# Kernel optimization log

Measured on AMD Instinct MI355X. Metric: run time of the kernel, lower is better.

Reference implementation:

```python
import jax, jax.numpy as jnp
from jax import lax
import numpy as np

B_SZ, L, NH, DH, DS = 2, 2048, 24, 64, 128


def setup_inputs() -> dict:
    key = jax.random.key(0)
    k1, k2, k3, k4 = jax.random.split(key, 4)
    x = jax.random.normal(k1, (B_SZ, L, NH, DH), dtype=jnp.float32)
    A = jax.random.normal(k2, (B_SZ, L, NH), dtype=jnp.float32)
    B_mat = jax.random.normal(k3, (B_SZ, L, NH, DS), dtype=jnp.float32)
    C_mat = jax.random.normal(k4, (B_SZ, L, NH, DS), dtype=jnp.float32)
    delta_param = jnp.zeros((NH,), dtype=jnp.float32)
    return {"x": x, "A": A, "B_mat": B_mat, "C_mat": C_mat, "delta_param": delta_param}


def reference(x, A, B_mat, C_mat, delta_param):
    # x: (B, L, nh, dh); A: (B, L, nh); B_mat/C_mat: (B, L, nh, ds)
    b, l, nh, dh = x.shape
    ds = B_mat.shape[-1]
    delta = jax.nn.softplus(A + delta_param[None, None, :])        # (B, L, nh)
    A_bar = jnp.exp(-delta * jnp.abs(A))                            # (B, L, nh)

    def step(h, inp):
        x_t, B_t, C_t, a_t = inp  # (B,nh,dh), (B,nh,ds), (B,nh,ds), (B,nh)
        h = a_t[:, :, None, None] * h + x_t[..., None] * B_t[:, :, None, :]
        y_t = jnp.einsum('bhds,bhs->bhd', h, C_t)                   # (B, nh, dh)
        return h, y_t

    h0 = jnp.zeros((b, nh, dh, ds), dtype=x.dtype)
    xs = (jnp.moveaxis(x, 1, 0),      # (L, B, nh, dh)
          jnp.moveaxis(B_mat, 1, 0),  # (L, B, nh, ds)
          jnp.moveaxis(C_mat, 1, 0),  # (L, B, nh, ds)
          jnp.moveaxis(A_bar, 1, 0))  # (L, B, nh)
    _, ys = lax.scan(step, h0, xs)    # ys: (L, B, nh, dh)
    return jnp.moveaxis(ys, 0, 1)     # (B, L, nh, dh)
```

## Files before the change

kernel.cpp:

```cpp
#include <hip/hip_runtime.h>

#define B_SZ 2
#define LSEQ 2048
#define NHh 24
#define DHh 64
#define DSs 128
#define TCH 64
#define NC  (LSEQ / TCH)
#define BH  (B_SZ * NHh)

#define S_ELEMS   (BH * LSEQ)
#define G_ELEMS   ((size_t)BH * NC * DSs * DHh)
#define WS_S_BYTES ((size_t)S_ELEMS * 4)
#define WS_G_BYTES (G_ELEMS * 2)
#define WS_REQ     (WS_S_BYTES + 2 * WS_G_BYTES)

#define SP  136
#define UP  72

typedef __attribute__((ext_vector_type(8))) short bf16x8;
typedef __attribute__((ext_vector_type(4))) float f32x4;

__device__ __forceinline__ unsigned short f2bf(float f) {
    union { float f; unsigned u; } v; v.f = f;
    unsigned r = ((v.u >> 16) & 1u) + 0x7FFFu;
    return (unsigned short)((v.u + r) >> 16);
}
__device__ __forceinline__ float bf2f(unsigned short h) {
    union { unsigned u; float f; } v; v.u = ((unsigned)h) << 16; return v.f;
}
__device__ __forceinline__ unsigned pk2(float a, float b) {
    return (unsigned)f2bf(a) | ((unsigned)f2bf(b) << 16);
}

__global__ __launch_bounds__(256, 3)
void k1_chunk(const float* __restrict__ x, const float* __restrict__ A,
              const float* __restrict__ Bm, const float* __restrict__ dp,
              float* __restrict__ S_ws, unsigned short* __restrict__ G_ws) {
    __shared__ __align__(16) union K1SM {
        struct {
            unsigned short bt[DSs][UP];
            unsigned short xt[DHh][UP];
            float          f[TCH];
        } a;
        unsigned short g[TCH][SP];
    } sm;

    const int c  = blockIdx.x & (NC - 1);
    const int bh = blockIdx.x >> 5;
    const int nh = bh % NHh; const int b = bh / NHh;
    const int tid = threadIdx.x;
    const int lane = tid & 63;
    const int w = tid >> 6;

    const size_t row0 = (size_t)(b * LSEQ + c * TCH) * NHh + nh;

    const int u = tid >> 2;
    const int q = tid & 3;
    const float* Brow = Bm + (row0 + (size_t)u * NHh) * DSs;
    const float* xrow = x  + (row0 + (size_t)u * NHh) * DHh;
    float4 bv[8], xv[4];
    #pragma unroll
    for (int j = 0; j < 8; ++j) bv[j] = *(const float4*)(Brow + (j * 4 + q) * 4);
    #pragma unroll
    for (int j = 0; j < 4; ++j) xv[j] = *(const float4*)(xrow + (j * 4 + q) * 4);

    #pragma unroll
    for (int j = 0; j < 8; ++j) {
        const int s = (j * 4 + q) * 4;
        sm.a.bt[s + 0][u] = f2bf(bv[j].x);
        sm.a.bt[s + 1][u] = f2bf(bv[j].y);
        sm.a.bt[s + 2][u] = f2bf(bv[j].z);
        sm.a.bt[s + 3][u] = f2bf(bv[j].w);
    }

    if (tid < 64) {
        float a  = A[row0 + (size_t)tid * NHh];
        float z  = a + dp[nh];
        float sp = (z > 20.0f) ? z : log1pf(expf(z));
        float la = -sp * fabsf(a);
        #pragma unroll
        for (int off = 1; off < 64; off <<= 1) {
            float v = __shfl_up(la, off, 64);
            if (lane >= off) la += v;
        }
        S_ws[(size_t)bh * LSEQ + c * TCH + tid] = la;
        float s63 = __shfl(la, 63, 64);
        sm.a.f[tid] = expf(s63 - la);
    }
    __syncthreads();

    const float f = sm.a.f[u];
    #pragma unroll
    for (int j = 0; j < 4; ++j) {
        const int d = (j * 4 + q) * 4;
        sm.a.xt[d + 0][u] = f2bf(xv[j].x * f);
        sm.a.xt[d + 1][u] = f2bf(xv[j].y * f);
        sm.a.xt[d + 2][u] = f2bf(xv[j].z * f);
        sm.a.xt[d + 3][u] = f2bf(xv[j].w * f);
    }
    __syncthreads();

    const int fr = lane >> 4, fc = lane & 15;
    bf16x8 afr0 = *(const bf16x8*)&sm.a.xt[16 * w + fc][fr * 8];
    bf16x8 afr1 = *(const bf16x8*)&sm.a.xt[16 * w + fc][32 + fr * 8];
    f32x4 accs[8];
    #pragma unroll
    for (int st = 0; st < 8; ++st) {
        f32x4 acc = {0.f, 0.f, 0.f, 0.f};
        bf16x8 b0 = *(const bf16x8*)&sm.a.bt[st * 16 + fc][fr * 8];
        bf16x8 b1 = *(const bf16x8*)&sm.a.bt[st * 16 + fc][32 + fr * 8];
        acc = __builtin_amdgcn_mfma_f32_16x16x32_bf16(afr0, b0, acc, 0, 0, 0);
        acc = __builtin_amdgcn_mfma_f32_16x16x32_bf16(afr1, b1, acc, 0, 0, 0);
        accs[st] = acc;
    }
    __syncthreads();

    #pragma unroll
    for (int st = 0; st < 8; ++st) {
        #pragma unroll
        for (int r = 0; r < 4; ++r)
            sm.g[16 * w + fr * 4 + r][st * 16 + fc] = f2bf(accs[st][r]);
    }
    __syncthreads();

    const int gr = tid >> 2;
    unsigned short* gbase = G_ws + (((size_t)bh * NC + c) * DHh + gr) * DSs;
    #pragma unroll
    for (int j = 0; j < 4; ++j) {
        const int s = (j * 4 + q) * 8;
        *(uint4*)(gbase + s) = *(const uint4*)&sm.g[gr][s];
    }
}

__global__ __launch_bounds__(64)
void k2_scan(const float* __restrict__ S_ws, const unsigned short* __restrict__ G_ws,
             unsigned short* __restrict__ H_ws) {
    const int dblk = blockIdx.x & 15;
    const int bh   = blockIdx.x >> 4;
    const int tid  = threadIdx.x;
    const int d    = dblk * 4 + (tid >> 4);
    const int s0   = (tid & 15) * 8;

    float h[8];
    #pragma unroll
    for (int k = 0; k < 8; ++k) h[k] = 0.f;

    size_t base = (((size_t)bh * NC) * DHh + d) * DSs + s0;
    const size_t cstride = (size_t)DHh * DSs;
    const float* Se = S_ws + (size_t)bh * LSEQ + (TCH - 1);

    uint4 g[16]; float sv[16];
    #pragma unroll
    for (int j = 0; j < 16; ++j) {
        g[j]  = *(const uint4*)(G_ws + base + (size_t)j * cstride);
        sv[j] = Se[(size_t)j * TCH];
    }
    #pragma unroll
    for (int c = 0; c < NC; c += 16) {
        #pragma unroll
        for (int j = 0; j < 16; ++j) {
            const int cc = c + j;
            uint4 p;
            p.x = pk2(h[0], h[1]); p.y = pk2(h[2], h[3]);
            p.z = pk2(h[4], h[5]); p.w = pk2(h[6], h[7]);
            *(uint4*)(H_ws + base + (size_t)cc * cstride) = p;
            const float e = expf(sv[j]);
            const unsigned gu[4] = {g[j].x, g[j].y, g[j].z, g[j].w};
            #pragma unroll
            for (int k = 0; k < 4; ++k) {
                h[2 * k]     = fmaf(e, h[2 * k],     bf2f((unsigned short)(gu[k] & 0xffff)));
                h[2 * k + 1] = fmaf(e, h[2 * k + 1], bf2f((unsigned short)(gu[k] >> 16)));
            }
            if (cc + 16 < NC) {
                g[j]  = *(const uint4*)(G_ws + base + (size_t)(cc + 16) * cstride);
                sv[j] = Se[(size_t)(cc + 16) * TCH];
            }
        }
    }
}

__global__ __launch_bounds__(256, 3)
void k3_y(const float* __restrict__ x, const float* __restrict__ Bm,
          const float* __restrict__ Cm, const float* __restrict__ S_ws,
          const unsigned short* __restrict__ H_ws, float* __restrict__ y) {
    __shared__ __align__(16) unsigned short sB[TCH * DSs];
    __shared__ __align__(16) unsigned short sH[DHh][SP];
    __shared__ __align__(16) unsigned short sW[TCH][UP];
    __shared__ __align__(16) unsigned short sXT[DHh][UP];
    __shared__ float sS[TCH];
    __shared__ float sEt[TCH];

    const int c  = blockIdx.x & (NC - 1);
    const int bh = blockIdx.x >> 5;
    const int nh = bh % NHh; const int b = bh / NHh;
    const int tid = threadIdx.x;
    const int lane = tid & 63;
    const int w = tid >> 6;
    const int fr = lane >> 4, fc = lane & 15;
    const int t0w = 16 * w;

    const size_t row0 = (size_t)(b * LSEQ + c * TCH) * NHh + nh;

    const int rr = tid >> 2;
    const int q  = tid & 3;
    const float* Brow = Bm + (row0 + (size_t)rr * NHh) * DSs;
    const float* xrow = x  + (row0 + (size_t)rr * NHh) * DHh;
    const unsigned short* Hrow = H_ws + (((size_t)bh * NC + c) * DHh + rr) * DSs;
    float4 bv[8], xv[4];
    uint4  hv[4];
    #pragma unroll
    for (int j = 0; j < 8; ++j) bv[j] = *(const float4*)(Brow + (j * 4 + q) * 4);
    #pragma unroll
    for (int j = 0; j < 4; ++j) xv[j] = *(const float4*)(xrow + (j * 4 + q) * 4);
    #pragma unroll
    for (int j = 0; j < 4; ++j) hv[j] = *(const uint4*)(Hrow + (j * 4 + q) * 8);

    const float* Cfr = Cm + (row0 + (size_t)(t0w + fc) * NHh) * DSs + fr * 8;
    float4 cf[8];
    #pragma unroll
    for (int kb = 0; kb < 4; ++kb) {
        cf[2 * kb]     = *(const float4*)(Cfr + kb * 32);
        cf[2 * kb + 1] = *(const float4*)(Cfr + kb * 32 + 4);
    }

    if (tid < 64) {
        float svv = S_ws[(size_t)bh * LSEQ + c * TCH + tid];
        sS[tid]  = svv;
        sEt[tid] = expf(svv);
    }

    bf16x8 ca[4];
    #pragma unroll
    for (int kb = 0; kb < 4; ++kb) {
        bf16x8 t;
        t[0] = (short)f2bf(cf[2 * kb].x);     t[1] = (short)f2bf(cf[2 * kb].y);
        t[2] = (short)f2bf(cf[2 * kb].z);     t[3] = (short)f2bf(cf[2 * kb].w);
        t[4] = (short)f2bf(cf[2 * kb + 1].x); t[5] = (short)f2bf(cf[2 * kb + 1].y);
        t[6] = (short)f2bf(cf[2 * kb + 1].z); t[7] = (short)f2bf(cf[2 * kb + 1].w);
        ca[kb] = t;
    }

    const int rsw = (rr & 15) << 3;
    #pragma unroll
    for (int j = 0; j < 8; ++j) {
        const int s = (j * 4 + q) * 4;
        *(uint2*)&sB[rr * DSs + (s ^ rsw)] =
            make_uint2(pk2(bv[j].x, bv[j].y), pk2(bv[j].z, bv[j].w));
    }
    #pragma unroll
    for (int j = 0; j < 4; ++j)
        *(uint4*)&sH[rr][(j * 4 + q) * 8] = hv[j];
    #pragma unroll
    for (int j = 0; j < 4; ++j) {
        const int d = (j * 4 + q) * 4;
        sXT[d + 0][rr] = f2bf(xv[j].x);
        sXT[d + 1][rr] = f2bf(xv[j].y);
        sXT[d + 2][rr] = f2bf(xv[j].z);
        sXT[d + 3][rr] = f2bf(xv[j].w);
    }
    __syncthreads();

    float st4[4];
    #pragma unroll
    for (int r = 0; r < 4; ++r) st4[r] = sS[t0w + fr * 4 + r];

    const int csw = fc << 3;
    #pragma unroll
    for (int ut = 0; ut < 4; ++ut) {
        const int u0 = ut * 16;
        unsigned short wv[4] = {0, 0, 0, 0};
        if (ut <= w) {
            f32x4 acc = {0.f, 0.f, 0.f, 0.f};
            #pragma unroll
            for (int kb = 0; kb < 4; ++kb) {
                bf16x8 bb = *(const bf16x8*)
                    &sB[(u0 + fc) * DSs + ((kb * 32 + fr * 8) ^ csw)];
                acc = __builtin_amdgcn_mfma_f32_16x16x32_bf16(ca[kb], bb, acc, 0, 0, 0);
            }
            const float su = sS[u0 + fc];
            const int   uu = u0 + fc;
            #pragma unroll
            for (int r = 0; r < 4; ++r) {
                const int t = t0w + fr * 4 + r;
                const float dd = fminf(st4[r] - su, 0.f);
                const float val = (uu <= t) ? acc[r] * expf(dd) : 0.f;
                wv[r] = f2bf(val);
            }
        }
        #pragma unroll
        for (int r = 0; r < 4; ++r) sW[t0w + fr * 4 + r][u0 + fc] = wv[r];
    }

    bf16x8 wa0 = *(const bf16x8*)&sW[t0w + fc][fr * 8];
    bf16x8 wa1;
    if (w >= 2) wa1 = *(const bf16x8*)&sW[t0w + fc][32 + fr * 8];
    float et4[4];
    #pragma unroll
    for (int r = 0; r < 4; ++r) et4[r] = sEt[t0w + fr * 4 + r];

    #pragma unroll
    for (int dt = 0; dt < 4; ++dt) {
        const int d0 = dt * 16;
        f32x4 acc = {0.f, 0.f, 0.f, 0.f};
        #pragma unroll
        for (int kb = 0; kb < 4; ++kb) {
            bf16x8 hb = *(const bf16x8*)&sH[d0 + fc][kb * 32 + fr * 8];
            acc = __builtin_amdgcn_mfma_f32_16x16x32_bf16(ca[kb], hb, acc, 0, 0, 0);
        }
        #pragma unroll
        for (int r = 0; r < 4; ++r) acc[r] *= et4[r];
        bf16x8 xb0 = *(const bf16x8*)&sXT[d0 + fc][fr * 8];
        acc = __builtin_amdgcn_mfma_f32_16x16x32_bf16(wa0, xb0, acc, 0, 0, 0);
        if (w >= 2) {
            bf16x8 xb1 = *(const bf16x8*)&sXT[d0 + fc][32 + fr * 8];
            acc = __builtin_amdgcn_mfma_f32_16x16x32_bf16(wa1, xb1, acc, 0, 0, 0);
        }
        float* yout = y + (row0 + (size_t)(t0w + fr * 4) * NHh) * DHh + d0 + fc;
        #pragma unroll
        for (int r = 0; r < 4; ++r) yout[(size_t)r * NHh * DHh] = acc[r];
    }
}

__device__ __forceinline__ void gload_lds16(const float* g, void* l) {
    __builtin_amdgcn_global_load_lds(
        (const __attribute__((address_space(1))) void*)g,
        (__attribute__((address_space(3))) void*)l, 16, 0, 0);
}
__device__ __forceinline__ void gload_lds4(const float* g, float* l) {
    __builtin_amdgcn_global_load_lds(
        (const __attribute__((address_space(1))) void*)g,
        (__attribute__((address_space(3))) void*)l, 4, 0, 0);
}
#define F_DBLK 4
#define F_DPW 16
#define F_TCH 32
#define F_NCH (LSEQ / F_TCH)
__global__ __launch_bounds__(256, 1)
void ssm_scan_fb(const float* __restrict__ x, const float* __restrict__ A,
                 const float* __restrict__ Bm, const float* __restrict__ Cm,
                 const float* __restrict__ dp, float* __restrict__ y) {
    __shared__ float s_abar[LSEQ];
    __shared__ float s_B[2][F_TCH][DSs];
    __shared__ float s_C[2][F_TCH][DSs];
    __shared__ float s_x[2][F_TCH][F_DPW];
    const int blk = blockIdx.x;
    const int dblk = blk % F_DBLK, bh = blk / F_DBLK;
    const int nh = bh % NHh, b = bh / NHh;
    const float dpv = dp[nh];
    for (int i = threadIdx.x; i < LSEQ; i += 256) {
        float a = A[(b * LSEQ + i) * NHh + nh];
        float z = a + dpv;
        float sp = (z > 20.0f) ? z : log1pf(expf(z));
        s_abar[i] = expf(-sp * fabsf(a));
    }
    const int tid = threadIdx.x, wid = tid >> 6, lane = tid & 63;
    const int dloc = tid >> 4, sg = tid & 15, sb = sg * 8;
    const size_t bh_off = (size_t)(b * LSEQ) * NHh + nh;
    const float* Bbase = Bm + bh_off * DSs;
    const float* Cbase = Cm + bh_off * DSs;
    const float* xbase = x + bh_off * DHh + dblk * F_DPW;
    float* yp = y + bh_off * DHh + dblk * F_DPW + dloc;
    const int RSTRIDE = NHh * DSs, XSTRIDE = NHh * DHh;
    auto stage = [&](int buf, int t0) {
        #pragma unroll
        for (int j = 0; j < 4; ++j) {
            const int r0 = (wid * 4 + j) * 2, r = r0 + (lane >> 5), col = (lane & 31) * 4;
            gload_lds16(Bbase + (size_t)(t0 + r) * RSTRIDE + col, &s_B[buf][r0][0]);
            gload_lds16(Cbase + (size_t)(t0 + r) * RSTRIDE + col, &s_C[buf][r0][0]);
        }
        #pragma unroll
        for (int j = 0; j < 2; ++j) {
            const int idx = (wid * 2 + j) * 64 + lane, t = idx >> 4, dc = idx & 15;
            gload_lds4(xbase + (size_t)(t0 + t) * XSTRIDE + dc, &s_x[buf][(wid * 2 + j) * 4][0]);
        }
    };
    stage(0, 0);
    __syncthreads();
    float h0=0,h1=0,h2=0,h3=0,h4=0,h5=0,h6=0,h7=0;
    for (int c = 0; c < F_NCH; ++c) {
        const int buf = c & 1;
        if (c + 1 < F_NCH) stage(buf ^ 1, (c + 1) * F_TCH);
        const int t0 = c * F_TCH;
        #pragma unroll 4
        for (int tt = 0; tt < F_TCH; ++tt) {
            const int t = t0 + tt;
            const float a = s_abar[t], xd = s_x[buf][tt][dloc];
            const float4* Br = (const float4*)&s_B[buf][tt][sb];
            const float4* Cr = (const float4*)&s_C[buf][tt][sb];
            const float4 B0 = Br[0], B1 = Br[1], C0 = Cr[0], C1 = Cr[1];
            h0 = fmaf(a, h0, xd * B0.x); h1 = fmaf(a, h1, xd * B0.y);
            h2 = fmaf(a, h2, xd * B0.z); h3 = fmaf(a, h3, xd * B0.w);
            h4 = fmaf(a, h4, xd * B1.x); h5 = fmaf(a, h5, xd * B1.y);
            h6 = fmaf(a, h6, xd * B1.z); h7 = fmaf(a, h7, xd * B1.w);
            float p0 = h0 * C0.x; p0 = fmaf(h1, C0.y, p0); p0 = fmaf(h2, C0.z, p0); p0 = fmaf(h3, C0.w, p0);
            float p1 = h4 * C1.x; p1 = fmaf(h5, C1.y, p1); p1 = fmaf(h6, C1.z, p1); p1 = fmaf(h7, C1.w, p1);
            float p = p0 + p1;
            p += __shfl_xor(p, 1, 64); p += __shfl_xor(p, 2, 64);
            p += __shfl_xor(p, 4, 64); p += __shfl_xor(p, 8, 64);
            if (sg == 0) yp[(size_t)t * XSTRIDE] = p;
        }
        __syncthreads();
    }
}

extern "C" void kernel_launch(void* const* d_in, const int* in_sizes, int n_in,
                              void* d_out, int out_size, void* d_ws, size_t ws_size,
                              hipStream_t stream) {
    const float* x  = (const float*)d_in[0];
    const float* A  = (const float*)d_in[1];
    const float* Bm = (const float*)d_in[2];
    const float* Cm = (const float*)d_in[3];
    const float* dp = (const float*)d_in[4];
    float* y = (float*)d_out;

    if (ws_size >= WS_REQ) {
        float* S_ws = (float*)d_ws;
        unsigned short* G_ws = (unsigned short*)((char*)d_ws + WS_S_BYTES);
        unsigned short* H_ws = G_ws + G_ELEMS;
        hipLaunchKernelGGL(k1_chunk, dim3(BH * NC), dim3(256), 0, stream,
                           x, A, Bm, dp, S_ws, G_ws);
        hipLaunchKernelGGL(k2_scan, dim3(BH * 16), dim3(64), 0, stream,
                           S_ws, G_ws, H_ws);
        hipLaunchKernelGGL(k3_y, dim3(BH * NC), dim3(256), 0, stream,
                           x, Bm, Cm, S_ws, H_ws, y);
    } else {
        hipLaunchKernelGGL(ssm_scan_fb, dim3(BH * F_DBLK), dim3(256), 0, stream,
                           x, A, Bm, Cm, dp, y);
    }
}
```

Baseline: 185.0 us.

## Fuse three-phase chunked scan into one cooperative kernel with grid syncs

Merges the chunk-state, inter-chunk scan and output kernels into a single cooperative launch of 768 blocks. Each block handles two chunks per phase, and two grid-wide syncs replace the kernel boundaries. This aims to remove launch gaps and tail effects between the three kernels. It trades them for grid-sync overhead, a shared-memory union that may lower occupancy, and the scan phase now running on 256-thread blocks. It falls back to the old three-kernel path if occupancy is too low or the launch fails.

```diff
diff --git a/kernel.cpp b/kernel.cpp
--- a/kernel.cpp
+++ b/kernel.cpp
@@ -1,4 +1,7 @@
 #include <hip/hip_runtime.h>
+#include <hip/hip_cooperative_groups.h>
+
+namespace cg = cooperative_groups;
 
 #define B_SZ 2
 #define LSEQ 2048
@@ -31,6 +34,281 @@
 }
 __device__ __forceinline__ unsigned pk2(float a, float b) {
     return (unsigned)f2bf(a) | ((unsigned)f2bf(b) << 16);
+}
+
+struct SMa {
+    unsigned short bt[DSs][UP];
+    unsigned short xt[DHh][UP];
+    float          f[TCH];
+    unsigned short g[TCH][SP];
+};
+struct SMb {
+    unsigned short sB[TCH * DSs];
+    unsigned short sH[DHh][SP];
+    unsigned short sW[TCH][UP];
+    unsigned short sXT[DHh][UP];
+    float sS[TCH];
+    float sEt[TCH];
+};
+union KSM { SMa a; SMb b; };
+
+__global__ __launch_bounds__(256, 3)
+void k_fused(const float* __restrict__ x, const float* __restrict__ A,
+             const float* __restrict__ Bm, const float* __restrict__ Cm,
+             const float* __restrict__ dp, float* __restrict__ S_ws,
+             unsigned short* __restrict__ G_ws, unsigned short* __restrict__ H_ws,
+             float* __restrict__ y) {
+    __shared__ __align__(16) KSM sm;
+
+    const int bid  = blockIdx.x;
+    const int bh   = bid >> 4;
+    const int ci   = bid & 15;
+    const int nh   = bh % NHh; const int b = bh / NHh;
+    const int tid  = threadIdx.x;
+    const int lane = tid & 63;
+    const int w    = tid >> 6;
+    const int fr   = lane >> 4, fc = lane & 15;
+
+    #pragma unroll 1
+    for (int cc = 0; cc < 2; ++cc) {
+        const int c = ci * 2 + cc;
+        __syncthreads();
+
+        const size_t row0 = (size_t)(b * LSEQ + c * TCH) * NHh + nh;
+        const int u = tid >> 2;
+        const int q = tid & 3;
+        const float* Brow = Bm + (row0 + (size_t)u * NHh) * DSs;
+        const float* xrow = x  + (row0 + (size_t)u * NHh) * DHh;
+        float4 bv[8], xv[4];
+        #pragma unroll
+        for (int j = 0; j < 8; ++j) bv[j] = *(const float4*)(Brow + (j * 4 + q) * 4);
+        #pragma unroll
+        for (int j = 0; j < 4; ++j) xv[j] = *(const float4*)(xrow + (j * 4 + q) * 4);
+
+        #pragma unroll
+        for (int j = 0; j < 8; ++j) {
+            const int s = (j * 4 + q) * 4;
+            sm.a.bt[s + 0][u] = f2bf(bv[j].x);
+            sm.a.bt[s + 1][u] = f2bf(bv[j].y);
+            sm.a.bt[s + 2][u] = f2bf(bv[j].z);
+            sm.a.bt[s + 3][u] = f2bf(bv[j].w);
+        }
+
+        if (tid < 64) {
+            float a  = A[row0 + (size_t)tid * NHh];
+            float z  = a + dp[nh];
+            float sp = (z > 20.0f) ? z : log1pf(expf(z));
+            float la = -sp * fabsf(a);
+            #pragma unroll
+            for (int off = 1; off < 64; off <<= 1) {
+                float v = __shfl_up(la, off, 64);
+                if (lane >= off) la += v;
+            }
+            S_ws[(size_t)bh * LSEQ + c * TCH + tid] = la;
+            float s63 = __shfl(la, 63, 64);
+            sm.a.f[tid] = expf(s63 - la);
+        }
+        __syncthreads();
+
+        const float f = sm.a.f[u];
+        #pragma unroll
+        for (int j = 0; j < 4; ++j) {
+            const int d = (j * 4 + q) * 4;
+            sm.a.xt[d + 0][u] = f2bf(xv[j].x * f);
+            sm.a.xt[d + 1][u] = f2bf(xv[j].y * f);
+            sm.a.xt[d + 2][u] = f2bf(xv[j].z * f);
+            sm.a.xt[d + 3][u] = f2bf(xv[j].w * f);
+        }
+        __syncthreads();
+
+        bf16x8 afr0 = *(const bf16x8*)&sm.a.xt[16 * w + fc][fr * 8];
+        bf16x8 afr1 = *(const bf16x8*)&sm.a.xt[16 * w + fc][32 + fr * 8];
+        #pragma unroll
+        for (int st = 0; st < 8; ++st) {
+            f32x4 acc = {0.f, 0.f, 0.f, 0.f};
+            bf16x8 b0 = *(const bf16x8*)&sm.a.bt[st * 16 + fc][fr * 8];
+            bf16x8 b1 = *(const bf16x8*)&sm.a.bt[st * 16 + fc][32 + fr * 8];
+            acc = __builtin_amdgcn_mfma_f32_16x16x32_bf16(afr0, b0, acc, 0, 0, 0);
+            acc = __builtin_amdgcn_mfma_f32_16x16x32_bf16(afr1, b1, acc, 0, 0, 0);
+            #pragma unroll
+            for (int r = 0; r < 4; ++r)
+                sm.a.g[16 * w + fr * 4 + r][st * 16 + fc] = f2bf(acc[r]);
+        }
+        __syncthreads();
+
+        const int gr = tid >> 2;
+        unsigned short* gbase = G_ws + (((size_t)bh * NC + c) * DHh + gr) * DSs;
+        #pragma unroll
+        for (int j = 0; j < 4; ++j) {
+            const int s = (j * 4 + q) * 8;
+            *(uint4*)(gbase + s) = *(const uint4*)&sm.a.g[gr][s];
+        }
+    }
+
+    cg::this_grid().sync();
+
+    {
+        const int unit = (bid << 2) | w;
+        const int sbh  = unit >> 6;
+        const int d    = unit & 63;
+        const int s0   = lane * 2;
+
+        float h0 = 0.f, h1 = 0.f;
+        size_t base = (((size_t)sbh * NC) * DHh + d) * DSs + s0;
+        const size_t cstride = (size_t)DHh * DSs;
+        const float* Se = S_ws + (size_t)sbh * LSEQ + (TCH - 1);
+
+        unsigned g[16]; float sv[16];
+        #pragma unroll
+        for (int j = 0; j < 16; ++j) {
+            g[j]  = *(const unsigned*)(G_ws + base + (size_t)j * cstride);
+            sv[j] = Se[(size_t)j * TCH];
+        }
+        #pragma unroll
+        for (int c = 0; c < NC; c += 16) {
+            #pragma unroll
+            for (int j = 0; j < 16; ++j) {
+                const int cc = c + j;
+                *(unsigned*)(H_ws + base + (size_t)cc * cstride) = pk2(h0, h1);
+                const float e = expf(sv[j]);
+                h0 = fmaf(e, h0, bf2f((unsigned short)(g[j] & 0xffff)));
+                h1 = fmaf(e, h1, bf2f((unsigned short)(g[j] >> 16)));
+                if (cc + 16 < NC) {
+                    g[j]  = *(const unsigned*)(G_ws + base + (size_t)(cc + 16) * cstride);
+                    sv[j] = Se[(size_t)(cc + 16) * TCH];
+                }
+            }
+        }
+    }
+
+    cg::this_grid().sync();
+
+    const int t0w = 16 * w;
+    #pragma unroll 1
+    for (int cc = 0; cc < 2; ++cc) {
+        const int c = ci * 2 + cc;
+        __syncthreads();
+
+        const size_t row0 = (size_t)(b * LSEQ + c * TCH) * NHh + nh;
+        const int rr = tid >> 2;
+        const int q  = tid & 3;
+        const float* Brow = Bm + (row0 + (size_t)rr * NHh) * DSs;
+        const float* xrow = x  + (row0 + (size_t)rr * NHh) * DHh;
+        const unsigned short* Hrow = H_ws + (((size_t)bh * NC + c) * DHh + rr) * DSs;
+        float4 bv[8], xv[4];
+        uint4  hv[4];
+        #pragma unroll
+        for (int j = 0; j < 8; ++j) bv[j] = *(const float4*)(Brow + (j * 4 + q) * 4);
+        #pragma unroll
+        for (int j = 0; j < 4; ++j) xv[j] = *(const float4*)(xrow + (j * 4 + q) * 4);
+        #pragma unroll
+        for (int j = 0; j < 4; ++j) hv[j] = *(const uint4*)(Hrow + (j * 4 + q) * 8);
+
+        const float* Cfr = Cm + (row0 + (size_t)(t0w + fc) * NHh) * DSs + fr * 8;
+        float4 cf[8];
+        #pragma unroll
+        for (int kb = 0; kb < 4; ++kb) {
+            cf[2 * kb]     = *(const float4*)(Cfr + kb * 32);
+            cf[2 * kb + 1] = *(const float4*)(Cfr + kb * 32 + 4);
+        }
+
+        if (tid < 64) {
+            float svv = S_ws[(size_t)bh * LSEQ + c * TCH + tid];
+            sm.b.sS[tid]  = svv;
+            sm.b.sEt[tid] = expf(svv);
+        }
+
+        bf16x8 ca[4];
+        #pragma unroll
+        for (int kb = 0; kb < 4; ++kb) {
+            bf16x8 t;
+            t[0] = (short)f2bf(cf[2 * kb].x);     t[1] = (short)f2bf(cf[2 * kb].y);
+            t[2] = (short)f2bf(cf[2 * kb].z);     t[3] = (short)f2bf(cf[2 * kb].w);
+            t[4] = (short)f2bf(cf[2 * kb + 1].x); t[5] = (short)f2bf(cf[2 * kb + 1].y);
+            t[6] = (short)f2bf(cf[2 * kb + 1].z); t[7] = (short)f2bf(cf[2 * kb + 1].w);
+            ca[kb] = t;
+        }
+
+        const int rsw = (rr & 15) << 3;
+        #pragma unroll
+        for (int j = 0; j < 8; ++j) {
+            const int s = (j * 4 + q) * 4;
+            *(uint2*)&sm.b.sB[rr * DSs + (s ^ rsw)] =
+                make_uint2(pk2(bv[j].x, bv[j].y), pk2(bv[j].z, bv[j].w));
+        }
+        #pragma unroll
+        for (int j = 0; j < 4; ++j)
+            *(uint4*)&sm.b.sH[rr][(j * 4 + q) * 8] = hv[j];
+        #pragma unroll
+        for (int j = 0; j < 4; ++j) {
+            const int d = (j * 4 + q) * 4;
+            sm.b.sXT[d + 0][rr] = f2bf(xv[j].x);
+            sm.b.sXT[d + 1][rr] = f2bf(xv[j].y);
+            sm.b.sXT[d + 2][rr] = f2bf(xv[j].z);
+            sm.b.sXT[d + 3][rr] = f2bf(xv[j].w);
+        }
+        __syncthreads();
+
+        float st4[4];
+        #pragma unroll
+        for (int r = 0; r < 4; ++r) st4[r] = sm.b.sS[t0w + fr * 4 + r];
+
+        const int csw = fc << 3;
+        #pragma unroll
+        for (int ut = 0; ut < 4; ++ut) {
+            const int u0 = ut * 16;
+            unsigned short wv[4] = {0, 0, 0, 0};
+            if (ut <= w) {
+                f32x4 acc = {0.f, 0.f, 0.f, 0.f};
+                #pragma unroll
+                for (int kb = 0; kb < 4; ++kb) {
+                    bf16x8 bb = *(const bf16x8*)
+                        &sm.b.sB[(u0 + fc) * DSs + ((kb * 32 + fr * 8) ^ csw)];
+                    acc = __builtin_amdgcn_mfma_f32_16x16x32_bf16(ca[kb], bb, acc, 0, 0, 0);
+                }
+                const float su = sm.b.sS[u0 + fc];
+                const int   uu = u0 + fc;
+                #pragma unroll
+                for (int r = 0; r < 4; ++r) {
+                    const int t = t0w + fr * 4 + r;
+                    const float dd = fminf(st4[r] - su, 0.f);
+                    const float val = (uu <= t) ? acc[r] * expf(dd) : 0.f;
+                    wv[r] = f2bf(val);
+                }
+            }
+            #pragma unroll
+            for (int r = 0; r < 4; ++r) sm.b.sW[t0w + fr * 4 + r][u0 + fc] = wv[r];
+        }
+
+        bf16x8 wa0 = *(const bf16x8*)&sm.b.sW[t0w + fc][fr * 8];
+        bf16x8 wa1;
+        if (w >= 2) wa1 = *(const bf16x8*)&sm.b.sW[t0w + fc][32 + fr * 8];
+        float et4[4];
+        #pragma unroll
+        for (int r = 0; r < 4; ++r) et4[r] = sm.b.sEt[t0w + fr * 4 + r];
+
+        #pragma unroll
+        for (int dt = 0; dt < 4; ++dt) {
+            const int d0 = dt * 16;
+            f32x4 acc = {0.f, 0.f, 0.f, 0.f};
+            #pragma unroll
+            for (int kb = 0; kb < 4; ++kb) {
+                bf16x8 hb = *(const bf16x8*)&sm.b.sH[d0 + fc][kb * 32 + fr * 8];
+                acc = __builtin_amdgcn_mfma_f32_16x16x32_bf16(ca[kb], hb, acc, 0, 0, 0);
+            }
+            #pragma unroll
+            for (int r = 0; r < 4; ++r) acc[r] *= et4[r];
+            bf16x8 xb0 = *(const bf16x8*)&sm.b.sXT[d0 + fc][fr * 8];
+            acc = __builtin_amdgcn_mfma_f32_16x16x32_bf16(wa0, xb0, acc, 0, 0, 0);
+            if (w >= 2) {
+                bf16x8 xb1 = *(const bf16x8*)&sm.b.sXT[d0 + fc][32 + fr * 8];
+                acc = __builtin_amdgcn_mfma_f32_16x16x32_bf16(wa1, xb1, acc, 0, 0, 0);
+            }
+            float* yout = y + (row0 + (size_t)(t0w + fr * 4) * NHh) * DHh + d0 + fc;
+            #pragma unroll
+            for (int r = 0; r < 4; ++r) yout[(size_t)r * NHh * DHh] = acc[r];
+        }
+    }
 }
 
 __global__ __launch_bounds__(256, 3)
@@ -54,7 +332,6 @@
     const int w = tid >> 6;
 
     const size_t row0 = (size_t)(b * LSEQ + c * TCH) * NHh + nh;
-
     const int u = tid >> 2;
     const int q = tid & 3;
     const float* Brow = Bm + (row0 + (size_t)u * NHh) * DSs;
@@ -201,7 +478,6 @@
     const int t0w = 16 * w;
 
     const size_t row0 = (size_t)(b * LSEQ + c * TCH) * NHh + nh;
-
     const int rr = tid >> 2;
     const int q  = tid & 3;
     const float* Brow = Bm + (row0 + (size_t)rr * NHh) * DSs;
@@ -418,6 +694,17 @@
         float* S_ws = (float*)d_ws;
         unsigned short* G_ws = (unsigned short*)((char*)d_ws + WS_S_BYTES);
         unsigned short* H_ws = G_ws + G_ELEMS;
+
+        int nb = 0;
+        hipError_t qe = hipOccupancyMaxActiveBlocksPerMultiprocessor(&nb, k_fused, 256, 0);
+        bool coop = (qe == hipSuccess) && (nb >= 3);
+        if (coop) {
+            void* args[] = {(void*)&x, (void*)&A, (void*)&Bm, (void*)&Cm, (void*)&dp,
+                            (void*)&S_ws, (void*)&G_ws, (void*)&H_ws, (void*)&y};
+            hipError_t le = hipLaunchCooperativeKernel((void*)k_fused, dim3(768), dim3(256),
+                                                       args, 0, stream);
+            if (le == hipSuccess) return;
+        }
         hipLaunchKernelGGL(k1_chunk, dim3(BH * NC), dim3(256), 0, stream,
                            x, A, Bm, dp, S_ws, G_ws);
         hipLaunchKernelGGL(k2_scan, dim3(BH * 16), dim3(64), 0, stream,
```

Result: no change. 184.7 us (-0.2%).

## Widen scan parallelism, alias LDS for B and H, raise occupancy bounds

Applied to the files above, without the earlier changes.

The inter-chunk scan kernel now gives each thread two state elements instead of eight, with one wave per d row. That quadruples the thread count, making far more loads and latency-bound recurrence chains run in parallel. k3 reuses a single swizzled LDS buffer for B and then H, separated by extra barriers, to cut shared memory so the raised launch bound of 4 blocks per SIMD can fit; k1's bound is also raised. The risks are register spills from the tighter bounds, extra barrier cost in k3, and narrower 4-byte accesses in the scan.

```diff
diff --git a/kernel.cpp b/kernel.cpp
--- a/kernel.cpp
+++ b/kernel.cpp
@@ -33,7 +33,7 @@
     return (unsigned)f2bf(a) | ((unsigned)f2bf(b) << 16);
 }
 
-__global__ __launch_bounds__(256, 3)
+__global__ __launch_bounds__(256, 4)
 void k1_chunk(const float* __restrict__ x, const float* __restrict__ A,
               const float* __restrict__ Bm, const float* __restrict__ dp,
               float* __restrict__ S_ws, unsigned short* __restrict__ G_ws) {
@@ -54,7 +54,6 @@
     const int w = tid >> 6;
 
     const size_t row0 = (size_t)(b * LSEQ + c * TCH) * NHh + nh;
-
     const int u = tid >> 2;
     const int q = tid & 3;
     const float* Brow = Bm + (row0 + (size_t)u * NHh) * DSs;
@@ -133,27 +132,25 @@
     }
 }
 
-__global__ __launch_bounds__(64)
+__global__ __launch_bounds__(256)
 void k2_scan(const float* __restrict__ S_ws, const unsigned short* __restrict__ G_ws,
              unsigned short* __restrict__ H_ws) {
-    const int dblk = blockIdx.x & 15;
-    const int bh   = blockIdx.x >> 4;
-    const int tid  = threadIdx.x;
-    const int d    = dblk * 4 + (tid >> 4);
-    const int s0   = (tid & 15) * 8;
-
-    float h[8];
-    #pragma unroll
-    for (int k = 0; k < 8; ++k) h[k] = 0.f;
-
+    const int w    = threadIdx.x >> 6;
+    const int lane = threadIdx.x & 63;
+    const int unit = (blockIdx.x << 2) | w;
+    const int bh   = unit >> 6;
+    const int d    = unit & 63;
+    const int s0   = lane * 2;
+
+    float h0 = 0.f, h1 = 0.f;
     size_t base = (((size_t)bh * NC) * DHh + d) * DSs + s0;
     const size_t cstride = (size_t)DHh * DSs;
     const float* Se = S_ws + (size_t)bh * LSEQ + (TCH - 1);
 
-    uint4 g[16]; float sv[16];
+    unsigned g[16]; float sv[16];
     #pragma unroll
     for (int j = 0; j < 16; ++j) {
-        g[j]  = *(const uint4*)(G_ws + base + (size_t)j * cstride);
+        g[j]  = *(const unsigned*)(G_ws + base + (size_t)j * cstride);
         sv[j] = Se[(size_t)j * TCH];
     }
     #pragma unroll
@@ -161,31 +158,23 @@
         #pragma unroll
         for (int j = 0; j < 16; ++j) {
             const int cc = c + j;
-            uint4 p;
-            p.x = pk2(h[0], h[1]); p.y = pk2(h[2], h[3]);
-            p.z = pk2(h[4], h[5]); p.w = pk2(h[6], h[7]);
-            *(uint4*)(H_ws + base + (size_t)cc * cstride) = p;
+            *(unsigned*)(H_ws + base + (size_t)cc * cstride) = pk2(h0, h1);
             const float e = expf(sv[j]);
-            const unsigned gu[4] = {g[j].x, g[j].y, g[j].z, g[j].w};
-            #pragma unroll
-            for (int k = 0; k < 4; ++k) {
-                h[2 * k]     = fmaf(e, h[2 * k],     bf2f((unsigned short)(gu[k] & 0xffff)));
-                h[2 * k + 1] = fmaf(e, h[2 * k + 1], bf2f((unsigned short)(gu[k] >> 16)));
-            }
+            h0 = fmaf(e, h0, bf2f((unsigned short)(g[j] & 0xffff)));
+            h1 = fmaf(e, h1, bf2f((unsigned short)(g[j] >> 16)));
             if (cc + 16 < NC) {
-                g[j]  = *(const uint4*)(G_ws + base + (size_t)(cc + 16) * cstride);
+                g[j]  = *(const unsigned*)(G_ws + base + (size_t)(cc + 16) * cstride);
                 sv[j] = Se[(size_t)(cc + 16) * TCH];
             }
         }
     }
 }
 
-__global__ __launch_bounds__(256, 3)
+__global__ __launch_bounds__(256, 4)
 void k3_y(const float* __restrict__ x, const float* __restrict__ Bm,
           const float* __restrict__ Cm, const float* __restrict__ S_ws,
           const unsigned short* __restrict__ H_ws, float* __restrict__ y) {
-    __shared__ __align__(16) unsigned short sB[TCH * DSs];
-    __shared__ __align__(16) unsigned short sH[DHh][SP];
+    __shared__ __align__(16) unsigned short sBH[TCH * DSs];
     __shared__ __align__(16) unsigned short sW[TCH][UP];
     __shared__ __align__(16) unsigned short sXT[DHh][UP];
     __shared__ float sS[TCH];
@@ -201,7 +190,6 @@
     const int t0w = 16 * w;
 
     const size_t row0 = (size_t)(b * LSEQ + c * TCH) * NHh + nh;
-
     const int rr = tid >> 2;
     const int q  = tid & 3;
     const float* Brow = Bm + (row0 + (size_t)rr * NHh) * DSs;
@@ -245,12 +233,9 @@
     #pragma unroll
     for (int j = 0; j < 8; ++j) {
         const int s = (j * 4 + q) * 4;
-        *(uint2*)&sB[rr * DSs + (s ^ rsw)] =
+        *(uint2*)&sBH[rr * DSs + (s ^ rsw)] =
             make_uint2(pk2(bv[j].x, bv[j].y), pk2(bv[j].z, bv[j].w));
     }
-    #pragma unroll
-    for (int j = 0; j < 4; ++j)
-        *(uint4*)&sH[rr][(j * 4 + q) * 8] = hv[j];
     #pragma unroll
     for (int j = 0; j < 4; ++j) {
         const int d = (j * 4 + q) * 4;
@@ -275,7 +260,7 @@
             #pragma unroll
             for (int kb = 0; kb < 4; ++kb) {
                 bf16x8 bb = *(const bf16x8*)
-                    &sB[(u0 + fc) * DSs + ((kb * 32 + fr * 8) ^ csw)];
+                    &sBH[(u0 + fc) * DSs + ((kb * 32 + fr * 8) ^ csw)];
                 acc = __builtin_amdgcn_mfma_f32_16x16x32_bf16(ca[kb], bb, acc, 0, 0, 0);
             }
             const float su = sS[u0 + fc];
@@ -292,6 +277,14 @@
         for (int r = 0; r < 4; ++r) sW[t0w + fr * 4 + r][u0 + fc] = wv[r];
     }
 
+    __syncthreads();
+    #pragma unroll
+    for (int j = 0; j < 4; ++j) {
+        const int s = (j * 4 + q) * 8;
+        *(uint4*)&sBH[rr * DSs + (s ^ rsw)] = hv[j];
+    }
+    __syncthreads();
+
     bf16x8 wa0 = *(const bf16x8*)&sW[t0w + fc][fr * 8];
     bf16x8 wa1;
     if (w >= 2) wa1 = *(const bf16x8*)&sW[t0w + fc][32 + fr * 8];
@@ -305,7 +298,8 @@
         f32x4 acc = {0.f, 0.f, 0.f, 0.f};
         #pragma unroll
         for (int kb = 0; kb < 4; ++kb) {
-            bf16x8 hb = *(const bf16x8*)&sH[d0 + fc][kb * 32 + fr * 8];
+            bf16x8 hb = *(const bf16x8*)
+                &sBH[(d0 + fc) * DSs + ((kb * 32 + fr * 8) ^ csw)];
             acc = __builtin_amdgcn_mfma_f32_16x16x32_bf16(ca[kb], hb, acc, 0, 0, 0);
         }
         #pragma unroll
@@ -420,7 +414,7 @@
         unsigned short* H_ws = G_ws + G_ELEMS;
         hipLaunchKernelGGL(k1_chunk, dim3(BH * NC), dim3(256), 0, stream,
                            x, A, Bm, dp, S_ws, G_ws);
-        hipLaunchKernelGGL(k2_scan, dim3(BH * 16), dim3(64), 0, stream,
+        hipLaunchKernelGGL(k2_scan, dim3(BH * 16), dim3(256), 0, stream,
                            S_ws, G_ws, H_ws);
         hipLaunchKernelGGL(k3_y, dim3(BH * NC), dim3(256), 0, stream,
                            x, Bm, Cm, S_ws, H_ws, y);
```

New measurement: 194.2 us. +4.9%, slower.
